# Kernel tuning notes

Measured on AMD Instinct MI355X. Metric: run time of the kernel, lower is better.

## Reference

```python
import jax, jax.numpy as jnp
import numpy as np

ALPHA = 0.01
EPSB = ALPHA / (1.0 - 2.0 * ALPHA)  # boundary_eps
BIG = 1e9  # stands in for +inf; all real boundary distances are << box diameter


def setup_inputs() -> dict:
    key = jax.random.key(0)
    ks = jax.random.split(key, 8)
    B, D, K = 32768, 16, 1024
    return {
        "x": jax.random.normal(ks[0], (B, D), jnp.float32),
        "logp": jnp.zeros((B, 1), jnp.float32),
        "an1_w": 0.1 * jax.random.normal(ks[1], (D,), jnp.float32),
        "an1_b": 0.1 * jax.random.normal(ks[2], (D,), jnp.float32),
        "an2_w": 0.1 * jax.random.normal(ks[3], (D,), jnp.float32),
        "an2_b": 0.1 * jax.random.normal(ks[4], (D,), jnp.float32),
        "shift_coeff": jax.random.normal(ks[5], (D,), jnp.float32),
        "anchor_raw": jax.random.normal(ks[6], (1, K, D), jnp.float32),  # vorproj._anchor_pts
        "box_min": -4.0 * jnp.ones((D,), jnp.float32),
        "box_max": 4.0 * jnp.ones((D,), jnp.float32),
        "mixture_logits": jnp.zeros((K,), jnp.float32),
    }


def reference(x, logp, an1_w, an1_b, an2_w, an2_b, shift_coeff,
              anchor_raw, box_min, box_max, mixture_logits):
    B, D = x.shape
    # --- actnorm1: y = (x + b) * exp(w); logdet = sum(w) ---
    x = (x + an1_b) * jnp.exp(an1_w)
    logp = logp - jnp.sum(an1_w)
    # --- logit_transform.inverse: y = (sigmoid(x) - alpha) / (1 - 2*alpha) ---
    ld = jnp.sum(jax.nn.log_sigmoid(x) + jax.nn.log_sigmoid(-x), axis=1, keepdims=True) \
         - D * jnp.log(1.0 - 2.0 * ALPHA)
    x = (jax.nn.sigmoid(x) - ALPHA) / (1.0 - 2.0 * ALPHA)
    logp = logp - ld
    # --- (-eps, 1+eps) -> (0, 1) ---
    span = 1.0 + 2.0 * EPSB
    x = (x + EPSB) / span
    logp = logp + D * jnp.log(span)
    # --- scale into box constraints ---
    scale = box_max - box_min  # (D,)
    x = x * scale + box_min
    logp = logp - jnp.sum(jnp.log(scale))
    # --- anchor points: R -> (-1,1) -> (0,1) -> box ---
    a = anchor_raw[0]                       # (K, D)
    a = a / (1.0 + jnp.abs(a))
    a = (a + 1.0) * 0.5 * scale + box_min   # (K, D)
    K = a.shape[0]
    # --- find_nearest: argmin_k ||x - a_k||^2 (drop const ||x||^2) ---
    a_sq = jnp.sum(a * a, axis=1)                    # (K,)
    d2 = a_sq[None, :] - 2.0 * (x @ a.T)             # (B, K)
    k = jnp.argmin(d2, axis=1)                       # (B,)
    mask = jax.nn.one_hot(k, K, dtype=bool).reshape(B, 1, K)
    x_k = a[k]                                       # (B, D) gathered anchor
    # --- shift toward anchor: x + c*(x_k - x); logdet = sum log(1-c) ---
    c = jax.nn.sigmoid(shift_coeff) * 0.98 + 0.01
    x = x + c * (x_k - x)
    logp = logp - jnp.sum(jnp.log1p(-c))
    # --- map_outside_cell: radial map of Voronoi cell (within box) onto R^D ---
    dx = x - x_k
    r = jnp.sqrt(jnp.sum(dx * dx, axis=1))           # (B,)
    u = dx / jnp.maximum(r, 1e-12)[:, None]          # (B, D) unit direction
    # half-plane boundary distance t_j = (||a_j - a_k||^2 / 2) / (u . (a_j - a_k))
    proj = u @ a.T - jnp.sum(u * x_k, axis=1, keepdims=True)              # (B, K)
    halfdist = 0.5 * (a_sq[None, :] + a_sq[k][:, None] - 2.0 * (x_k @ a.T))  # (B, K)
    self_mask = jnp.arange(K)[None, :] == k[:, None]
    valid = jnp.logical_and(jnp.logical_not(self_mask), proj > 1e-12)
    t_half = jnp.where(valid, halfdist / jnp.where(valid, proj, 1.0), BIG)
    # box-face distances along u
    up = u > 1e-12
    un = u < -1e-12
    t_box = jnp.where(up, (box_max[None, :] - x_k) / jnp.where(up, u, 1.0),
            jnp.where(un, (box_min[None, :] - x_k) / jnp.where(un, u, 1.0), BIG))
    t = jnp.minimum(jnp.min(t_half, axis=1), jnp.min(t_box, axis=1))      # (B,)
    ratio = r / t                                     # in [0, 0.99] after shift
    s = 1.0 / (1.0 - ratio)
    x = x_k + dx * s[:, None]
    # logdet = (D+1) * log(t / (t - r)) = -(D+1) * log1p(-ratio)
    logp = logp + (D + 1.0) * jnp.log1p(-ratio)[:, None]
    # --- subtract cell center ---
    x = x - x_k
    # --- actnorm2 ---
    x = (x + an2_b) * jnp.exp(an2_w)
    logp = logp - jnp.sum(an2_w)
    # --- mixture component log-prob ---
    logprobs = jax.nn.log_softmax(mixture_logits)
    logp = logp - logprobs[k][:, None]
    return x, logp, mask
```

## Files before the change

kernel.cpp:

```cpp
#include <hip/hip_runtime.h>
#include <math.h>

#define DD 16
#define KK 1024

#define WS_A    0
#define WS_ASQ  16384
#define WS_OMC  17408
#define WS_B2   17424
#define WS_E2   17440
#define WS_MN   17456
#define WS_MX   17472
#define WS_SCL  17488
#define WS_DIM  17504
#define WS_E1   17520
#define WS_BASE 17536
#define WS_TOTD 17537
#define WS_NEED_BYTES (WS_TOTD * 8)

__device__ __forceinline__ double xformD(double rv, double mn, double scl) {
  double t = rv / (1.0 + fabs(rv));
  return (t + 1.0) * 0.5 * scl + mn;
}
__device__ __forceinline__ float xformF(float v, float mn, float mx) {
  return (v / (1.f + fabsf(v)) + 1.f) * 0.5f * (mx - mn) + mn;
}

__global__ __launch_bounds__(256) void vor_pre(
    const float* __restrict__ an1_w, const float* __restrict__ an2_w,
    const float* __restrict__ an2_b, const float* __restrict__ shift_c,
    const float* __restrict__ anchor_raw,
    const float* __restrict__ box_min, const float* __restrict__ box_max,
    const float* __restrict__ mlogits, double* __restrict__ ws)
{
  __shared__ double redD[16];
  const int tid = threadIdx.x;
  const int blk = blockIdx.x;

  if (blk == 0 && tid < DD) {
    double w1 = (double)an1_w[tid], w2 = (double)an2_w[tid];
    double sgc = 1.0 / (1.0 + exp(-(double)shift_c[tid]));
    double c = sgc * 0.98 + 0.01;
    double mn = (double)box_min[tid], mx = (double)box_max[tid];
    ws[WS_OMC + tid] = 1.0 - c;
    ws[WS_B2  + tid] = (double)an2_b[tid];
    ws[WS_E2  + tid] = exp(w2);
    ws[WS_MN  + tid] = mn;
    ws[WS_MX  + tid] = mx;
    ws[WS_SCL + tid] = mx - mn;
    ws[WS_E1  + tid] = exp(w1);
    ws[WS_DIM + tid] = -w1 - log(mx - mn) - log1p(-c) - w2;
  }
  const int j0 = blk * 64;
  for (int e = tid; e < 64 * DD; e += 256) {
    int j = j0 + (e >> 4), d = e & 15;
    double mn = (double)box_min[d];
    double scl = (double)box_max[d] - mn;
    ws[WS_A + (size_t)j * DD + d] = xformD((double)anchor_raw[j * DD + d], mn, scl);
  }
  __syncthreads();
  for (int j = j0 + tid; j < j0 + 64; j += 256) {
    double s = 0.0;
    #pragma unroll
    for (int d = 0; d < DD; ++d) { double a = ws[WS_A + (size_t)j * DD + d]; s = fma(a, a, s); }
    ws[WS_ASQ + j] = s;
  }
  if (blk != 0) return;
  float lm = -3.4e38f;
  for (int i = tid; i < KK; i += 256) lm = fmaxf(lm, mlogits[i]);
  #pragma unroll
  for (int o = 32; o > 0; o >>= 1) lm = fmaxf(lm, __shfl_xor(lm, o));
  if ((tid & 63) == 0) redD[tid >> 6] = (double)lm;
  __syncthreads();
  float gmax = (float)fmax(fmax(redD[0], redD[1]), fmax(redD[2], redD[3]));
  double lsum = 0.0;
  for (int i = tid; i < KK; i += 256) lsum += exp((double)mlogits[i] - (double)gmax);
  #pragma unroll
  for (int o = 32; o > 0; o >>= 1) lsum += __shfl_xor(lsum, o);
  if ((tid & 63) == 0) redD[4 + (tid >> 6)] = lsum;
  __syncthreads();
  if (tid == 0) {
    double lse = (double)gmax + log(redD[4] + redD[5] + redD[6] + redD[7]);
    double b = (double)DD * (log(0.98) + log(1.0 + 2.0 * (0.01 / 0.98)));
    #pragma unroll
    for (int d = 0; d < DD; ++d) b += ws[WS_DIM + d];
    ws[WS_BASE] = b + lse;
  }
}

#define NT2 1024
#define RPB2 128
#define SL2 8
#define JSL2 (KK / SL2)

__global__ __launch_bounds__(NT2, 4) void vor3(
    const float* __restrict__ x_in, const float* __restrict__ logp_in,
    const float* __restrict__ an1_b,
    const float* __restrict__ mlogits, const double* __restrict__ ws,
    float* __restrict__ out, int Brows)
{
  __shared__ __align__(16) float sA[KK][DD];
  __shared__ float  sAsqH[KK];
  __shared__ double sD2[16][64];
  __shared__ int    sJJ[16][64];
  __shared__ float  sRat[16][64];
  __shared__ float  sOmcF[DD], sB2F[DD], sE2F[DD], sMnF[DD], sMxF[DD];

  const int tid  = threadIdx.x;
  const int w    = tid >> 6;
  const int lane = tid & 63;
  const int rg   = w >> 3;
  const int sl   = w & 7;
  const int rrow = rg * 64 + lane;
  const int row  = blockIdx.x * RPB2 + rrow;
  const size_t coreEnd = (size_t)Brows * (DD + 1);

  if (tid < DD) {
    sOmcF[tid] = (float)ws[WS_OMC + tid];
    sB2F[tid]  = (float)ws[WS_B2 + tid];
    sE2F[tid]  = (float)ws[WS_E2 + tid];
    sMnF[tid]  = (float)ws[WS_MN + tid];
    sMxF[tid]  = (float)ws[WS_MX + tid];
  }
  for (int e = tid; e < KK * DD / 4; e += NT2) {
    double2 p0 = ((const double2*)(ws + WS_A))[e * 2 + 0];
    double2 p1 = ((const double2*)(ws + WS_A))[e * 2 + 1];
    ((float4*)sA)[e] = make_float4((float)p0.x, (float)p0.y, (float)p1.x, (float)p1.y);
  }
  __syncthreads();
  for (int j = tid; j < KK; j += NT2) {
    float acc = 0.f;
    #pragma unroll
    for (int d = 0; d < DD; ++d) { float a = sA[j][d]; acc = fmaf(a, a, acc); }
    sAsqH[j] = 0.5f * acc;
  }
  {
    float4* mz = (float4*)(out + coreEnd + (size_t)blockIdx.x * RPB2 * KK);
    #pragma unroll 4
    for (int i = tid; i < RPB2 * KK / 4; i += NT2)
      mz[i] = make_float4(0.f, 0.f, 0.f, 0.f);
  }

  const double A = 0.01, EPSB = 0.01 / 0.98;
  const double SPAN = 1.0 + 2.0 * EPSB;
  double x4d[DD];
  float  x4f[DD];
  double lsigD = 0.0;
  {
    const float* xr = x_in + (size_t)row * DD;
    #pragma unroll
    for (int d = 0; d < DD; ++d) {
      double y1 = ((double)xr[d] + (double)an1_b[d]) * ws[WS_E1 + d];
      double sg = 1.0 / (1.0 + exp(-y1));
      double x2 = (sg - A) / (1.0 - 2.0 * A);
      double x3 = (x2 + EPSB) / SPAN;
      double x4 = x3 * ws[WS_SCL + d] + ws[WS_MN + d];
      x4d[d] = x4;
      x4f[d] = (float)x4;
      if (sl == 0) {
        double ay = fabs(y1);
        lsigD += ay + 2.0 * log1p(exp(-ay));
      }
    }
  }
  __syncthreads();

  const int jlo = sl * JSL2, jhi = jlo + JSL2;
  float m1 = -3.4e38f, m2v = -3.4e38f;
  int j1 = jlo, j2v = jlo;
  #pragma unroll 2
  for (int j = jlo; j < jhi; ++j) {
    float acc = -sAsqH[j];
    const float4* ar = (const float4*)&sA[j][0];
    #pragma unroll
    for (int dq = 0; dq < 4; ++dq) {
      float4 a4 = ar[dq];
      acc = fmaf(x4f[4 * dq + 0], a4.x, acc);
      acc = fmaf(x4f[4 * dq + 1], a4.y, acc);
      acc = fmaf(x4f[4 * dq + 2], a4.z, acc);
      acc = fmaf(x4f[4 * dq + 3], a4.w, acc);
    }
    bool gt1 = acc > m1;
    bool gt2 = acc > m2v;
    m2v = gt1 ? m1 : (gt2 ? acc : m2v);
    j2v = gt1 ? j1 : (gt2 ? j : j2v);
    m1  = gt1 ? acc : m1;
    j1  = gt1 ? j : j1;
  }

  {
    double bestD = 1e300; int bk = 0x7fffffff;
    #pragma unroll
    for (int t = 0; t < 2; ++t) {
      int j = t ? j2v : j1;
      const double* aj = ws + WS_A + (size_t)j * DD;
      double dot = 0.0;
      #pragma unroll
      for (int d = 0; d < DD; ++d) dot = fma(x4d[d], aj[d], dot);
      double d2 = ws[WS_ASQ + j] - 2.0 * dot;
      if (d2 < bestD || (d2 == bestD && j < bk)) { bestD = d2; bk = j; }
    }
    sD2[w][lane] = bestD;
    sJJ[w][lane] = bk;
  }
  __syncthreads();

  int k = 0x7fffffff;
  {
    double kb = 1e300;
    #pragma unroll
    for (int ss = 0; ss < SL2; ++ss) {
      double d = sD2[rg * 8 + ss][lane];
      int    j = sJJ[rg * 8 + ss][lane];
      if (d < kb || (d == kb && j < k)) { kb = d; k = j; }
    }
  }

  float akf[DD], dxf[DD];
  float r2f = 0.f, dxak = 0.f;
  #pragma unroll
  for (int d = 0; d < DD; ++d) {
    float a = sA[k][d];
    akf[d] = a;
    float dx = sOmcF[d] * (x4f[d] - a);
    dxf[d] = dx;
    r2f  = fmaf(dx, dx, r2f);
    dxak = fmaf(dx, a, dxak);
  }
  const float rf   = sqrtf(r2f);
  const float rrf  = fmaxf(rf, 1e-12f);
  const float scal = rf / rrf;
  const float epsr = 1e-12f * rf;
  const float asqhk = sAsqH[k];

  float q1 = 0.f, h1 = 1.f;
  #pragma unroll 2
  for (int j = jlo; j < jhi; ++j) {
    float q = -dxak;
    float h = asqhk + sAsqH[j];
    const float4* ar = (const float4*)&sA[j][0];
    #pragma unroll
    for (int dq = 0; dq < 4; ++dq) {
      float4 a4 = ar[dq];
      q = fmaf(dxf[4 * dq + 0], a4.x, q);
      q = fmaf(dxf[4 * dq + 1], a4.y, q);
      q = fmaf(dxf[4 * dq + 2], a4.z, q);
      q = fmaf(dxf[4 * dq + 3], a4.w, q);
      h = fmaf(-akf[4 * dq + 0], a4.x, h);
      h = fmaf(-akf[4 * dq + 1], a4.y, h);
      h = fmaf(-akf[4 * dq + 2], a4.z, h);
      h = fmaf(-akf[4 * dq + 3], a4.w, h);
    }
    bool upd = (j != k) & (q > epsr) & (q * h1 > q1 * h);
    q1 = upd ? q : q1;
    h1 = upd ? h : h1;
  }
  sRat[w][lane] = scal * (q1 / h1);
  __syncthreads();

  if (sl == 0) {
    float ratio = rf * 1e-9f;
    #pragma unroll
    for (int ss = 0; ss < SL2; ++ss) ratio = fmaxf(ratio, sRat[rg * 8 + ss][lane]);
    #pragma unroll
    for (int d = 0; d < DD; ++d) {
      float uf = dxf[d] / rrf;
      if (uf > 1e-12f)        ratio = fmaxf(ratio, rf * uf / (sMxF[d] - akf[d]));
      else if (uf < -1e-12f)  ratio = fmaxf(ratio, rf * uf / (sMnF[d] - akf[d]));
    }
    float sS = 1.0f / (1.0f - ratio);
    float xo[DD];
    #pragma unroll
    for (int d = 0; d < DD; ++d)
      xo[d] = (dxf[d] * sS + sB2F[d]) * sE2F[d];
    float4* xp = (float4*)(out + (size_t)row * DD);
    xp[0] = make_float4(xo[0], xo[1], xo[2], xo[3]);
    xp[1] = make_float4(xo[4], xo[5], xo[6], xo[7]);
    xp[2] = make_float4(xo[8], xo[9], xo[10], xo[11]);
    xp[3] = make_float4(xo[12], xo[13], xo[14], xo[15]);
    double lp = (double)logp_in[row] + ws[WS_BASE] + lsigD
              + 17.0 * log1p(-(double)ratio)
              - (double)mlogits[k];
    out[(size_t)Brows * DD + row] = (float)lp;
    out[coreEnd + (size_t)row * KK + k] = 1.0f;
  }
}

#define NT 256
#define RPB 64
#define SLC4 4
#define JSL4 (KK / SLC4)

__global__ __launch_bounds__(NT, 2) void vor_green(
    const float* __restrict__ x_in, const float* __restrict__ logp_in,
    const float* __restrict__ an1_w, const float* __restrict__ an1_b,
    const float* __restrict__ an2_w, const float* __restrict__ an2_b,
    const float* __restrict__ shift_c, const float* __restrict__ anchor_raw,
    const float* __restrict__ box_min, const float* __restrict__ box_max,
    const float* __restrict__ mlogits,
    float* __restrict__ out, int Brows)
{
  __shared__ __align__(16) float sA[KK][DD];
  __shared__ float  sAsqH[KK];
  __shared__ float  sX4T[DD][RPB];
  __shared__ int    sPj1[SLC4][RPB], sPj2[SLC4][RPB];
  __shared__ int    sRI1[SLC4][RPB], sRI2[SLC4][RPB];
  __shared__ double sPartD[8];
  __shared__ double sE1D[DD], sB1D[DD], sOmcD[DD], sB2D[DD], sE2D[DD];
  __shared__ double sMnD[DD], sMxD[DD], sSclD[DD], sDimD[DD];
  __shared__ double sBaseD;
  __shared__ int    sKidx[RPB];

  const int tid  = threadIdx.x;
  const int sl   = tid >> 6;
  const int lane = tid & 63;
  const int row  = blockIdx.x * RPB + lane;
  const size_t coreEnd = (size_t)Brows * (DD + 1);

  for (int e = tid; e < KK * DD / 4; e += NT) {
    float4 raw = ((const float4*)anchor_raw)[e];
    float4 bmn = ((const float4*)box_min)[e & 3];
    float4 bmx = ((const float4*)box_max)[e & 3];
    float4 o;
    o.x = xformF(raw.x, bmn.x, bmx.x);
    o.y = xformF(raw.y, bmn.y, bmx.y);
    o.z = xformF(raw.z, bmn.z, bmx.z);
    o.w = xformF(raw.w, bmn.w, bmx.w);
    ((float4*)sA)[e] = o;
  }
  if (tid < DD) {
    double w1 = (double)an1_w[tid];
    sE1D[tid] = exp(w1);
    sB1D[tid] = (double)an1_b[tid];
    double sgc = 1.0 / (1.0 + exp(-(double)shift_c[tid]));
    double c = sgc * 0.98 + 0.01;
    sOmcD[tid] = 1.0 - c;
    double mn = (double)box_min[tid], mx = (double)box_max[tid];
    sMnD[tid] = mn; sMxD[tid] = mx; sSclD[tid] = mx - mn;
    double w2 = (double)an2_w[tid];
    sE2D[tid] = exp(w2);
    sB2D[tid] = (double)an2_b[tid];
    sDimD[tid] = -w1 - log(mx - mn) - log1p(-c) - w2;
  }
  __syncthreads();

  for (int j = tid; j < KK; j += NT) {
    float acc = 0.f;
    #pragma unroll
    for (int d = 0; d < DD; ++d) { float a = sA[j][d]; acc = fmaf(a, a, acc); }
    sAsqH[j] = 0.5f * acc;
  }

  float lm = -3.4e38f;
  for (int i = tid; i < KK; i += NT) lm = fmaxf(lm, mlogits[i]);
  #pragma unroll
  for (int o = 32; o > 0; o >>= 1) lm = fmaxf(lm, __shfl_xor(lm, o));
  if (lane == 0) sPartD[sl] = (double)lm;
  __syncthreads();
  float gmax = (float)fmax(fmax(sPartD[0], sPartD[1]), fmax(sPartD[2], sPartD[3]));
  double lsum = 0.0;
  for (int i = tid; i < KK; i += NT) lsum += exp((double)mlogits[i] - (double)gmax);
  #pragma unroll
  for (int o = 32; o > 0; o >>= 1) lsum += __shfl_xor(lsum, o);
  if (lane == 0) sPartD[4 + sl] = lsum;
  __syncthreads();
  if (tid == 0) {
    double lse = (double)gmax + log(sPartD[4] + sPartD[5] + sPartD[6] + sPartD[7]);
    double b = (double)DD * (log(0.98) + log(1.0 + 2.0 * (0.01 / 0.98)));
    #pragma unroll
    for (int d = 0; d < DD; ++d) b += sDimD[d];
    sBaseD = b + lse;
  }

  double x4d[DD];
  double lsigD = 0.0;
  if (sl == 0) {
    const double A = 0.01, EPSB = 0.01 / 0.98;
    const double SPAN = 1.0 + 2.0 * EPSB;
    const float* xr = x_in + (size_t)row * DD;
    #pragma unroll
    for (int d = 0; d < DD; ++d) {
      double y1 = ((double)xr[d] + sB1D[d]) * sE1D[d];
      double sg = 1.0 / (1.0 + exp(-y1));
      double x2 = (sg - A) / (1.0 - 2.0 * A);
      double x3 = (x2 + EPSB) / SPAN;
      double x4 = x3 * sSclD[d] + sMnD[d];
      x4d[d] = x4;
      sX4T[d][lane] = (float)x4;
      double ay = fabs(y1);
      lsigD += ay + 2.0 * log1p(exp(-ay));
    }
  }
  {
    float4* mz = (float4*)(out + coreEnd + (size_t)blockIdx.x * RPB * KK);
    #pragma unroll 4
    for (int i = tid; i < RPB * KK / 4; i += NT)
      mz[i] = make_float4(0.f, 0.f, 0.f, 0.f);
  }
  __syncthreads();

  float x4f[DD];
  #pragma unroll
  for (int d = 0; d < DD; ++d) x4f[d] = sX4T[d][lane];

  float m1 = -3.4e38f, m2v = -3.4e38f;
  int j1 = 0x7fffffff, j2v = 0x7fffffff;
  const int jlo = sl * JSL4, jhi = jlo + JSL4;
  #pragma unroll 2
  for (int j = jlo; j < jhi; ++j) {
    float acc = -sAsqH[j];
    const float4* ar = (const float4*)&sA[j][0];
    #pragma unroll
    for (int dq = 0; dq < 4; ++dq) {
      float4 a4 = ar[dq];
      acc = fmaf(x4f[4 * dq + 0], a4.x, acc);
      acc = fmaf(x4f[4 * dq + 1], a4.y, acc);
      acc = fmaf(x4f[4 * dq + 2], a4.z, acc);
      acc = fmaf(x4f[4 * dq + 3], a4.w, acc);
    }
    bool gt1 = acc > m1;
    bool gt2 = acc > m2v;
    m2v = gt1 ? m1 : (gt2 ? acc : m2v);
    j2v = gt1 ? j1 : (gt2 ? j : j2v);
    m1  = gt1 ? acc : m1;
    j1  = gt1 ? j : j1;
  }
  sPj1[sl][lane] = j1;
  sPj2[sl][lane] = j2v;
  __syncthreads();

  if (sl == 0) {
    double best = 1e300; int bk = 0x7fffffff;
    #pragma unroll
    for (int ss = 0; ss < SLC4; ++ss) {
      #pragma unroll
      for (int t = 0; t < 2; ++t) {
        int j = t ? sPj2[ss][lane] : sPj1[ss][lane];
        double asq = 0.0, dot = 0.0;
        #pragma unroll
        for (int d = 0; d < DD; ++d) {
          double a = xformD((double)anchor_raw[j * DD + d], sMnD[d], sSclD[d]);
          asq = fma(a, a, asq);
          dot = fma(x4d[d], a, dot);
        }
        double d2 = asq - 2.0 * dot;
        if (d2 < best || (d2 == best && j < bk)) { best = d2; bk = j; }
      }
    }
    sKidx[lane] = bk;
  }
  __syncthreads();

  const int k = sKidx[lane];

  float akf[DD], dxf[DD];
  float r2f = 0.f, dxak = 0.f;
  #pragma unroll
  for (int d = 0; d < DD; ++d) {
    float a = sA[k][d];
    akf[d] = a;
    float dx = (float)sOmcD[d] * (x4f[d] - a);
    dxf[d] = dx;
    r2f  = fmaf(dx, dx, r2f);
    dxak = fmaf(dx, a, dxak);
  }
  const float epsr = 1e-12f * sqrtf(r2f);
  const float asqhk = sAsqH[k];

  float q1 = 0.f, h1 = 1.f, q2 = 0.f, h2 = 1.f;
  int i1 = -1, i2 = -1;
  #pragma unroll 2
  for (int j = jlo; j < jhi; ++j) {
    float q = -dxak;
    float h = asqhk + sAsqH[j];
    const float4* ar = (const float4*)&sA[j][0];
    #pragma unroll
    for (int dq = 0; dq < 4; ++dq) {
      float4 a4 = ar[dq];
      q = fmaf(dxf[4 * dq + 0], a4.x, q);
      q = fmaf(dxf[4 * dq + 1], a4.y, q);
      q = fmaf(dxf[4 * dq + 2], a4.z, q);
      q = fmaf(dxf[4 * dq + 3], a4.w, q);
      h = fmaf(-akf[4 * dq + 0], a4.x, h);
      h = fmaf(-akf[4 * dq + 1], a4.y, h);
      h = fmaf(-akf[4 * dq + 2], a4.z, h);
      h = fmaf(-akf[4 * dq + 3], a4.w, h);
    }
    bool valid = (j != k) & (q > epsr);
    bool b1 = valid && (q * h1 > q1 * h);
    bool b2 = valid && (q * h2 > q2 * h);
    float nq2 = b1 ? q1 : (b2 ? q : q2);
    float nh2 = b1 ? h1 : (b2 ? h : h2);
    int   ni2 = b1 ? i1 : (b2 ? j : i2);
    q1 = b1 ? q : q1; h1 = b1 ? h : h1; i1 = b1 ? j : i1;
    q2 = nq2; h2 = nh2; i2 = ni2;
  }
  sRI1[sl][lane] = i1;
  sRI2[sl][lane] = i2;
  __syncthreads();

  if (sl == 0) {
    double akD[DD], dxD[DD];
    double r2 = 0.0;
    #pragma unroll
    for (int d = 0; d < DD; ++d) {
      double a = xformD((double)anchor_raw[k * DD + d], sMnD[d], sSclD[d]);
      akD[d] = a;
      double dx = sOmcD[d] * (x4d[d] - a);
      dxD[d] = dx;
      r2 = fma(dx, dx, r2);
    }
    double rD = sqrt(r2);
    double rr = fmax(rD, 1e-12);
    double ratio = rD / 1e9;

    #pragma unroll
    for (int ss = 0; ss < SLC4; ++ss) {
      #pragma unroll
      for (int t = 0; t < 2; ++t) {
        int j = t ? sRI2[ss][lane] : sRI1[ss][lane];
        if (j < 0 || j == k) continue;
        double q = 0.0, h = 0.0;
        #pragma unroll
        for (int d = 0; d < DD; ++d) {
          double aj = xformD((double)anchor_raw[j * DD + d], sMnD[d], sSclD[d]);
          double g = aj - akD[d];
          q = fma(dxD[d], g, q);
          h = fma(g, g, h);
        }
        double proj = q / rr;
        if (proj > 1e-12) {
          double cand = rD * proj / (0.5 * h);
          ratio = fmax(ratio, cand);
        }
      }
    }
    #pragma unroll
    for (int d = 0; d < DD; ++d) {
      double u = dxD[d] / rr;
      if (u > 1e-12)        ratio = fmax(ratio, rD * u / (sMxD[d] - akD[d]));
      else if (u < -1e-12)  ratio = fmax(ratio, rD * u / (sMnD[d] - akD[d]));
    }

    double sS = 1.0 / (1.0 - ratio);
    float* xo = out + (size_t)row * DD;
    #pragma unroll
    for (int d = 0; d < DD; ++d) {
      double x7 = dxD[d] * sS;
      double x8 = (x7 + sB2D[d]) * sE2D[d];
      xo[d] = (float)x8;
    }
    double lp = (double)logp_in[row] + sBaseD + lsigD
              + 17.0 * log1p(-ratio)
              - (double)mlogits[k];
    out[(size_t)Brows * DD + row] = (float)lp;
    out[coreEnd + (size_t)row * KK + k] = 1.0f;
  }
}

extern "C" void kernel_launch(void* const* d_in, const int* in_sizes, int n_in,
                              void* d_out, int out_size, void* d_ws, size_t ws_size,
                              hipStream_t stream) {
  (void)n_in; (void)out_size;
  const float* x_in   = (const float*)d_in[0];
  const float* logp   = (const float*)d_in[1];
  const float* an1w   = (const float*)d_in[2];
  const float* an1b   = (const float*)d_in[3];
  const float* an2w   = (const float*)d_in[4];
  const float* an2b   = (const float*)d_in[5];
  const float* shiftc = (const float*)d_in[6];
  const float* anchor = (const float*)d_in[7];
  const float* bmin   = (const float*)d_in[8];
  const float* bmax   = (const float*)d_in[9];
  const float* mlog   = (const float*)d_in[10];
  const int B = in_sizes[0] / DD;

  if (ws_size >= (size_t)WS_NEED_BYTES && d_ws != nullptr && (B % RPB2) == 0) {
    double* ws = (double*)d_ws;
    hipLaunchKernelGGL(vor_pre, dim3(16), dim3(256), 0, stream,
                       an1w, an2w, an2b, shiftc, anchor, bmin, bmax, mlog, ws);
    hipLaunchKernelGGL(vor3, dim3(B / RPB2), dim3(NT2), 0, stream,
                       x_in, logp, an1b, mlog,
                       (const double*)ws, (float*)d_out, B);
  } else {
    hipLaunchKernelGGL(vor_green, dim3(B / RPB), dim3(NT), 0, stream,
                       x_in, logp, an1w, an1b, an2w, an2b, shiftc, anchor,
                       bmin, bmax, mlog, (float*)d_out, B);
  }
}
```

Baseline: 111.1 us.

## Compute per-row input transform once per block in shared memory and split FMA chains

The double-precision sigmoid/logit input transform was previously done redundantly by all 8 slice-warps per row; now each (row, dim) element is computed once cooperatively and stored in shared memory, with the log-sigmoid terms stored too. The inner dot-product loops are split into two independent accumulator chains to shorten FMA dependency latency, and the first scan is unrolled by 4. This costs extra shared memory (about 24KB), which may reduce occupancy, and the log-sigmoid sum now accumulates in float instead of double.

Measured after the change: 104.2 us. -6.2%, faster.

```diff
diff --git a/kernel.cpp b/kernel.cpp
--- a/kernel.cpp
+++ b/kernel.cpp
@@ -93,7 +93,7 @@
 #define SL2 8
 #define JSL2 (KK / SL2)
 
-__global__ __launch_bounds__(NT2, 4) void vor3(
+__global__ __launch_bounds__(NT2, 4) void vor4(
     const float* __restrict__ x_in, const float* __restrict__ logp_in,
     const float* __restrict__ an1_b,
     const float* __restrict__ mlogits, const double* __restrict__ ws,
@@ -101,6 +101,8 @@
 {
   __shared__ __align__(16) float sA[KK][DD];
   __shared__ float  sAsqH[KK];
+  __shared__ double sX4D[DD][RPB2];
+  __shared__ float  sLT[DD][RPB2];
   __shared__ double sD2[16][64];
   __shared__ int    sJJ[16][64];
   __shared__ float  sRat[16][64];
@@ -127,12 +129,21 @@
     double2 p1 = ((const double2*)(ws + WS_A))[e * 2 + 1];
     ((float4*)sA)[e] = make_float4((float)p0.x, (float)p0.y, (float)p1.x, (float)p1.y);
   }
-  __syncthreads();
-  for (int j = tid; j < KK; j += NT2) {
-    float acc = 0.f;
-    #pragma unroll
-    for (int d = 0; d < DD; ++d) { float a = sA[j][d]; acc = fmaf(a, a, acc); }
-    sAsqH[j] = 0.5f * acc;
+  {
+    const double A = 0.01, EPSB = 0.01 / 0.98;
+    const double SPAN = 1.0 + 2.0 * EPSB;
+    const float* xb = x_in + (size_t)blockIdx.x * RPB2 * DD;
+    for (int e = tid; e < RPB2 * DD; e += NT2) {
+      int rr = e >> 4, d = e & 15;
+      double y1 = ((double)xb[e] + (double)an1_b[d]) * ws[WS_E1 + d];
+      double sg = 1.0 / (1.0 + exp(-y1));
+      double x2 = (sg - A) / (1.0 - 2.0 * A);
+      double x3 = (x2 + EPSB) / SPAN;
+      double x4 = x3 * ws[WS_SCL + d] + ws[WS_MN + d];
+      sX4D[d][rr] = x4;
+      double ay = fabs(y1);
+      sLT[d][rr] = (float)(ay + 2.0 * log1p(exp(-ay)));
+    }
   }
   {
     float4* mz = (float4*)(out + coreEnd + (size_t)blockIdx.x * RPB2 * KK);
@@ -140,46 +151,37 @@
     for (int i = tid; i < RPB2 * KK / 4; i += NT2)
       mz[i] = make_float4(0.f, 0.f, 0.f, 0.f);
   }
-
-  const double A = 0.01, EPSB = 0.01 / 0.98;
-  const double SPAN = 1.0 + 2.0 * EPSB;
-  double x4d[DD];
-  float  x4f[DD];
-  double lsigD = 0.0;
-  {
-    const float* xr = x_in + (size_t)row * DD;
-    #pragma unroll
-    for (int d = 0; d < DD; ++d) {
-      double y1 = ((double)xr[d] + (double)an1_b[d]) * ws[WS_E1 + d];
-      double sg = 1.0 / (1.0 + exp(-y1));
-      double x2 = (sg - A) / (1.0 - 2.0 * A);
-      double x3 = (x2 + EPSB) / SPAN;
-      double x4 = x3 * ws[WS_SCL + d] + ws[WS_MN + d];
-      x4d[d] = x4;
-      x4f[d] = (float)x4;
-      if (sl == 0) {
-        double ay = fabs(y1);
-        lsigD += ay + 2.0 * log1p(exp(-ay));
-      }
-    }
-  }
+  __syncthreads();
+
+  for (int j = tid; j < KK; j += NT2) {
+    float acc = 0.f;
+    #pragma unroll
+    for (int d = 0; d < DD; ++d) { float a = sA[j][d]; acc = fmaf(a, a, acc); }
+    sAsqH[j] = 0.5f * acc;
+  }
+
+  float x4f[DD];
+  #pragma unroll
+  for (int d = 0; d < DD; ++d) x4f[d] = (float)sX4D[d][rrow];
   __syncthreads();
 
   const int jlo = sl * JSL2, jhi = jlo + JSL2;
   float m1 = -3.4e38f, m2v = -3.4e38f;
   int j1 = jlo, j2v = jlo;
-  #pragma unroll 2
+  #pragma unroll 4
   for (int j = jlo; j < jhi; ++j) {
-    float acc = -sAsqH[j];
     const float4* ar = (const float4*)&sA[j][0];
-    #pragma unroll
-    for (int dq = 0; dq < 4; ++dq) {
-      float4 a4 = ar[dq];
-      acc = fmaf(x4f[4 * dq + 0], a4.x, acc);
-      acc = fmaf(x4f[4 * dq + 1], a4.y, acc);
-      acc = fmaf(x4f[4 * dq + 2], a4.z, acc);
-      acc = fmaf(x4f[4 * dq + 3], a4.w, acc);
-    }
+    float4 a0 = ar[0], a1 = ar[1], a2 = ar[2], a3 = ar[3];
+    float accA = -sAsqH[j], accB = 0.f;
+    accA = fmaf(x4f[0],  a0.x, accA); accB = fmaf(x4f[8],  a2.x, accB);
+    accA = fmaf(x4f[1],  a0.y, accA); accB = fmaf(x4f[9],  a2.y, accB);
+    accA = fmaf(x4f[2],  a0.z, accA); accB = fmaf(x4f[10], a2.z, accB);
+    accA = fmaf(x4f[3],  a0.w, accA); accB = fmaf(x4f[11], a2.w, accB);
+    accA = fmaf(x4f[4],  a1.x, accA); accB = fmaf(x4f[12], a3.x, accB);
+    accA = fmaf(x4f[5],  a1.y, accA); accB = fmaf(x4f[13], a3.y, accB);
+    accA = fmaf(x4f[6],  a1.z, accA); accB = fmaf(x4f[14], a3.z, accB);
+    accA = fmaf(x4f[7],  a1.w, accA); accB = fmaf(x4f[15], a3.w, accB);
+    float acc = accA + accB;
     bool gt1 = acc > m1;
     bool gt2 = acc > m2v;
     m2v = gt1 ? m1 : (gt2 ? acc : m2v);
@@ -196,7 +198,7 @@
       const double* aj = ws + WS_A + (size_t)j * DD;
       double dot = 0.0;
       #pragma unroll
-      for (int d = 0; d < DD; ++d) dot = fma(x4d[d], aj[d], dot);
+      for (int d = 0; d < DD; ++d) dot = fma(sX4D[d][rrow], aj[d], dot);
       double d2 = ws[WS_ASQ + j] - 2.0 * dot;
       if (d2 < bestD || (d2 == bestD && j < bk)) { bestD = d2; bk = j; }
     }
@@ -236,21 +238,27 @@
   float q1 = 0.f, h1 = 1.f;
   #pragma unroll 2
   for (int j = jlo; j < jhi; ++j) {
-    float q = -dxak;
-    float h = asqhk + sAsqH[j];
     const float4* ar = (const float4*)&sA[j][0];
-    #pragma unroll
-    for (int dq = 0; dq < 4; ++dq) {
-      float4 a4 = ar[dq];
-      q = fmaf(dxf[4 * dq + 0], a4.x, q);
-      q = fmaf(dxf[4 * dq + 1], a4.y, q);
-      q = fmaf(dxf[4 * dq + 2], a4.z, q);
-      q = fmaf(dxf[4 * dq + 3], a4.w, q);
-      h = fmaf(-akf[4 * dq + 0], a4.x, h);
-      h = fmaf(-akf[4 * dq + 1], a4.y, h);
-      h = fmaf(-akf[4 * dq + 2], a4.z, h);
-      h = fmaf(-akf[4 * dq + 3], a4.w, h);
-    }
+    float4 a0 = ar[0], a1 = ar[1], a2 = ar[2], a3 = ar[3];
+    float qA = -dxak, qB = 0.f;
+    float hA = asqhk + sAsqH[j], hB = 0.f;
+    qA = fmaf(dxf[0],  a0.x, qA); qB = fmaf(dxf[8],  a2.x, qB);
+    hA = fmaf(-akf[0], a0.x, hA); hB = fmaf(-akf[8], a2.x, hB);
+    qA = fmaf(dxf[1],  a0.y, qA); qB = fmaf(dxf[9],  a2.y, qB);
+    hA = fmaf(-akf[1], a0.y, hA); hB = fmaf(-akf[9], a2.y, hB);
+    qA = fmaf(dxf[2],  a0.z, qA); qB = fmaf(dxf[10], a2.z, qB);
+    hA = fmaf(-akf[2], a0.z, hA); hB = fmaf(-akf[10],a2.z, hB);
+    qA = fmaf(dxf[3],  a0.w, qA); qB = fmaf(dxf[11], a2.w, qB);
+    hA = fmaf(-akf[3], a0.w, hA); hB = fmaf(-akf[11],a2.w, hB);
+    qA = fmaf(dxf[4],  a1.x, qA); qB = fmaf(dxf[12], a3.x, qB);
+    hA = fmaf(-akf[4], a1.x, hA); hB = fmaf(-akf[12],a3.x, hB);
+    qA = fmaf(dxf[5],  a1.y, qA); qB = fmaf(dxf[13], a3.y, qB);
+    hA = fmaf(-akf[5], a1.y, hA); hB = fmaf(-akf[13],a3.y, hB);
+    qA = fmaf(dxf[6],  a1.z, qA); qB = fmaf(dxf[14], a3.z, qB);
+    hA = fmaf(-akf[6], a1.z, hA); hB = fmaf(-akf[14],a3.z, hB);
+    qA = fmaf(dxf[7],  a1.w, qA); qB = fmaf(dxf[15], a3.w, qB);
+    hA = fmaf(-akf[7], a1.w, hA); hB = fmaf(-akf[15],a3.w, hB);
+    float q = qA + qB, h = hA + hB;
     bool upd = (j != k) & (q > epsr) & (q * h1 > q1 * h);
     q1 = upd ? q : q1;
     h1 = upd ? h : h1;
@@ -270,15 +278,18 @@
     }
     float sS = 1.0f / (1.0f - ratio);
     float xo[DD];
-    #pragma unroll
-    for (int d = 0; d < DD; ++d)
+    float lsig = 0.f;
+    #pragma unroll
+    for (int d = 0; d < DD; ++d) {
       xo[d] = (dxf[d] * sS + sB2F[d]) * sE2F[d];
+      lsig += sLT[d][rrow];
+    }
     float4* xp = (float4*)(out + (size_t)row * DD);
     xp[0] = make_float4(xo[0], xo[1], xo[2], xo[3]);
     xp[1] = make_float4(xo[4], xo[5], xo[6], xo[7]);
     xp[2] = make_float4(xo[8], xo[9], xo[10], xo[11]);
     xp[3] = make_float4(xo[12], xo[13], xo[14], xo[15]);
-    double lp = (double)logp_in[row] + ws[WS_BASE] + lsigD
+    double lp = (double)logp_in[row] + ws[WS_BASE] + (double)lsig
               + 17.0 * log1p(-(double)ratio)
               - (double)mlogits[k];
     out[(size_t)Brows * DD + row] = (float)lp;
@@ -579,7 +590,7 @@
     double* ws = (double*)d_ws;
     hipLaunchKernelGGL(vor_pre, dim3(16), dim3(256), 0, stream,
                        an1w, an2w, an2b, shiftc, anchor, bmin, bmax, mlog, ws);
-    hipLaunchKernelGGL(vor3, dim3(B / RPB2), dim3(NT2), 0, stream,
+    hipLaunchKernelGGL(vor4, dim3(B / RPB2), dim3(NT2), 0, stream,
                        x_in, logp, an1b, mlog,
                        (const double*)ws, (float*)d_out, B);
   } else {
```
